# Kernel tuning notes

Measured on AMD Instinct MI355X. Metric: run time of the kernel, lower is better.

Reference implementation:

```python
import jax, jax.numpy as jnp
import numpy as np

B, T, D, N = 2, 2048, 1024, 16
DT_RANK = 64  # ceil(D / 16)


def setup_inputs() -> dict:
    key = jax.random.key(0)
    ks = jax.random.split(key, 8)
    x = jax.random.normal(ks[0], (B, T, D), dtype=jnp.float32)
    # Linear weights stored as (out, in) like torch; applied as x @ W.T
    W_B = jax.random.normal(ks[1], (N, D), dtype=jnp.float32) / np.sqrt(D)
    W_C = jax.random.normal(ks[2], (N, D), dtype=jnp.float32) / np.sqrt(D)
    W_dt1 = jax.random.normal(ks[3], (DT_RANK, D), dtype=jnp.float32) / np.sqrt(D)
    W_dt2 = jax.random.normal(ks[4], (D, DT_RANK), dtype=jnp.float32) / np.sqrt(DT_RANK)
    # dt bias init: inverse-softplus of dt sampled log-uniform in [dt_min, dt_max]
    dt_min, dt_max = 1e-3, 1e-1
    u = jax.random.uniform(ks[5], (D,), dtype=jnp.float32)
    dt_init = jnp.clip(jnp.exp(u * (np.log(dt_max) - np.log(dt_min)) + np.log(dt_min)), 1e-4, None)
    b_dt2 = dt_init + jnp.log(-jnp.expm1(-dt_init))
    # log_A: per original non-HiPPO path, A in (0.5, 1.0), broadcast to (D, N)
    a = jax.random.uniform(ks[6], (N,), dtype=jnp.float32) * 0.5 + 0.5
    log_A = jnp.broadcast_to(jnp.log(a)[None, :], (D, N)).copy()
    D_skip = jnp.ones((D,), dtype=jnp.float32)
    return {"x": x, "W_B": W_B, "W_C": W_C, "W_dt1": W_dt1,
            "W_dt2": W_dt2, "b_dt2": b_dt2, "log_A": log_A, "D_skip": D_skip}


def _selective_scan(A_bar, B_bar, C):
    # A_bar, B_bar: (B, T, D, N); C: (B, T, N) -> y: (B, T, D)
    def step(h, inputs):
        a_t, b_t, c_t = inputs  # (B,D,N), (B,D,N), (B,N)
        h = a_t * h + b_t
        y_t = jnp.einsum('bdn,bn->bd', h, c_t)
        return h, y_t

    h0 = jnp.zeros(A_bar.shape[:1] + A_bar.shape[2:], dtype=A_bar.dtype)  # (B,D,N)
    xs = (jnp.moveaxis(A_bar, 1, 0), jnp.moveaxis(B_bar, 1, 0), jnp.moveaxis(C, 1, 0))
    _, ys = jax.lax.scan(step, h0, xs)  # ys: (T, B, D)
    return jnp.moveaxis(ys, 0, 1)


def reference(x, W_B, W_C, W_dt1, W_dt2, b_dt2, log_A, D_skip):
    # Projections
    B_t = jnp.einsum('btd,nd->btn', x, W_B)          # (B,T,N)
    C_t = jnp.einsum('btd,nd->btn', x, W_C)          # (B,T,N)
    dt_raw = jnp.einsum('btr,dr->btd', jnp.einsum('btd,rd->btr', x, W_dt1), W_dt2) + b_dt2
    dt = jax.nn.softplus(dt_raw)                     # (B,T,D)
    A = -jnp.exp(log_A)                              # (D,N), negative
    # Discretization
    A_bar = jnp.exp(dt[..., None] * A[None, None])   # (B,T,D,N)
    dB = (A_bar - 1.0) / (A[None, None] + 1e-8)
    B_bar = dB * x[..., None] * B_t[:, :, None, :]   # (B,T,D,N)
    y = _selective_scan(A_bar, B_bar, C_t)           # (B,T,D)
    return y + D_skip * x
```

## Files before the change

### kernel.cpp

```cpp
#include <hip/hip_runtime.h>
#include <hip/hip_bf16.h>

#define BB 2
#define TT 2048
#define DD 1024
#define NN 16
#define RR 64
#define MM (BB*TT)
#define KDIM DD
#define CHUNK 64
#define NCHUNK (TT/CHUNK)

#define BT_OFF 0
#define CT_OFF 65536
#define R1_OFF 131072
#define DT_OFF 393216
#define P_OFF  4587520
#define S_OFF  5636096

__device__ __forceinline__ float softplus_f(float z) {
    return fmaxf(z, 0.0f) + log1pf(expf(-fabsf(z)));
}

__global__ __launch_bounds__(256) void k_proj96(
    const float* __restrict__ x, const float* __restrict__ W_B,
    const float* __restrict__ W_C, const float* __restrict__ W_dt1,
    float* __restrict__ Bt, float* __restrict__ Ct, float* __restrict__ R1)
{
    __shared__ float xs[16][68];
    __shared__ float wsT[16][97];

    const int tid = threadIdx.x;
    const int r0 = blockIdx.x * 64;
    const int kbase = blockIdx.y * 256;
    const int tx = tid & 15;
    const int ty = tid >> 4;

    float acc[4][6];
    #pragma unroll
    for (int i = 0; i < 4; i++)
        #pragma unroll
        for (int j = 0; j < 6; j++) acc[i][j] = 0.0f;

    for (int kc = 0; kc < 256; kc += 16) {
        {
            const int row = tid >> 2;
            const int kq = (tid & 3) * 4;
            float4 v = *(const float4*)(x + (size_t)(r0 + row) * KDIM + kbase + kc + kq);
            xs[kq + 0][row] = v.x; xs[kq + 1][row] = v.y;
            xs[kq + 2][row] = v.z; xs[kq + 3][row] = v.w;
        }
        #pragma unroll
        for (int i = 0; i < 6; i++) {
            const int idx = i * 256 + tid;
            const int c = idx >> 4;
            const int kk = idx & 15;
            const float* wrow; int cc;
            if (c < 16)      { wrow = W_B;   cc = c; }
            else if (c < 32) { wrow = W_C;   cc = c - 16; }
            else             { wrow = W_dt1; cc = c - 32; }
            wsT[kk][c] = wrow[(size_t)cc * KDIM + kbase + kc + kk];
        }
        __syncthreads();
        #pragma unroll
        for (int kk = 0; kk < 16; kk++) {
            const float a0 = xs[kk][ty * 4 + 0];
            const float a1 = xs[kk][ty * 4 + 1];
            const float a2 = xs[kk][ty * 4 + 2];
            const float a3 = xs[kk][ty * 4 + 3];
            #pragma unroll
            for (int j = 0; j < 6; j++) {
                const float b = wsT[kk][tx + j * 16];
                acc[0][j] = fmaf(a0, b, acc[0][j]);
                acc[1][j] = fmaf(a1, b, acc[1][j]);
                acc[2][j] = fmaf(a2, b, acc[2][j]);
                acc[3][j] = fmaf(a3, b, acc[3][j]);
            }
        }
        __syncthreads();
    }

    #pragma unroll
    for (int i = 0; i < 4; i++) {
        const int r = r0 + ty * 4 + i;
        #pragma unroll
        for (int j = 0; j < 6; j++) {
            const int c = tx + j * 16;
            const float v = acc[i][j];
            if (c < 16)      atomicAdd(&Bt[r * NN + c], v);
            else if (c < 32) atomicAdd(&Ct[r * NN + (c - 16)], v);
            else             atomicAdd(&R1[r * RR + (c - 32)], v);
        }
    }
}

__global__ __launch_bounds__(256) void k_dtproj(
    const float* __restrict__ R1, const float* __restrict__ W_dt2,
    const float* __restrict__ b_dt2, float* __restrict__ dt)
{
    __shared__ float r1s[16][65];
    __shared__ float wsT[64][256];

    const int tid = threadIdx.x;
    const int r0 = blockIdx.x * 16;
    const int d0 = blockIdx.y * 256;

    {
        const int row = tid >> 4;
        const int kq = (tid & 15) * 4;
        float4 v = *(const float4*)(R1 + (size_t)(r0 + row) * RR + kq);
        r1s[row][kq + 0] = v.x; r1s[row][kq + 1] = v.y;
        r1s[row][kq + 2] = v.z; r1s[row][kq + 3] = v.w;
    }
    {
        const float* src = W_dt2 + (size_t)(d0 + tid) * RR;
        #pragma unroll
        for (int kq = 0; kq < 64; kq += 4) {
            float4 v = *(const float4*)(src + kq);
            wsT[kq + 0][tid] = v.x; wsT[kq + 1][tid] = v.y;
            wsT[kq + 2][tid] = v.z; wsT[kq + 3][tid] = v.w;
        }
    }
    __syncthreads();

    const int r = tid & 15;
    const int dg = tid >> 4;

    float4 acc[4];
    #pragma unroll
    for (int q = 0; q < 4; q++) acc[q] = make_float4(0.f, 0.f, 0.f, 0.f);

    #pragma unroll 4
    for (int k = 0; k < 64; k++) {
        const float a = r1s[r][k];
        #pragma unroll
        for (int q = 0; q < 4; q++) {
            float4 bv = *(const float4*)&wsT[k][dg * 16 + q * 4];
            acc[q].x = fmaf(a, bv.x, acc[q].x);
            acc[q].y = fmaf(a, bv.y, acc[q].y);
            acc[q].z = fmaf(a, bv.z, acc[q].z);
            acc[q].w = fmaf(a, bv.w, acc[q].w);
        }
    }

    float* out = dt + (size_t)(r0 + r) * DD + d0 + dg * 16;
    const float* bb = b_dt2 + d0 + dg * 16;
    #pragma unroll
    for (int q = 0; q < 4; q++) {
        float4 bias = *(const float4*)(bb + q * 4);
        float4 o;
        o.x = softplus_f(acc[q].x + bias.x);
        o.y = softplus_f(acc[q].y + bias.y);
        o.z = softplus_f(acc[q].z + bias.z);
        o.w = softplus_f(acc[q].w + bias.w);
        *(float4*)(out + q * 4) = o;
    }
}

__global__ __launch_bounds__(256) void k_scan1(
    const float* __restrict__ x, const float* __restrict__ dt,
    const float* __restrict__ Bt, const float* __restrict__ log_A,
    float* __restrict__ P, float* __restrict__ S)
{
    __shared__ float dt_s[CHUNK][64];
    __shared__ float x_s[CHUNK][64];
    __shared__ float bt_s[CHUNK][NN];

    const int tid = threadIdx.x;
    const int ng = tid & 3;
    const int dl = tid >> 2;
    const int d0 = blockIdx.x * 64;
    const int d  = d0 + dl;
    const int c  = blockIdx.y;
    const int b  = blockIdx.z;
    const int n0 = ng * 4;
    const int base = b * TT + c * CHUNK;

    {
        const float* gdt = dt + (size_t)base * DD + d0;
        const float* gx  = x  + (size_t)base * DD + d0;
        #pragma unroll
        for (int k = 0; k < 4; k++) {
            const int f = tid + k * 256;
            const int t = f >> 4;
            const int j = (f & 15) * 4;
            *(float4*)&dt_s[t][j] = *(const float4*)(gdt + (size_t)t * DD + j);
            *(float4*)&x_s[t][j]  = *(const float4*)(gx  + (size_t)t * DD + j);
        }
        const float* gbt = Bt + (size_t)base * NN;
        const int t = tid >> 2;
        const int j = (tid & 3) * 4;
        *(float4*)&bt_s[t][j] = *(const float4*)(gbt + (size_t)t * NN + j);
    }

    const float4 lg = *(const float4*)(log_A + d * NN + n0);
    const float A0 = -__expf(lg.x), A1 = -__expf(lg.y),
                A2 = -__expf(lg.z), A3 = -__expf(lg.w);
    const float rA0 = 1.0f / (A0 + 1e-8f), rA1 = 1.0f / (A1 + 1e-8f),
                rA2 = 1.0f / (A2 + 1e-8f), rA3 = 1.0f / (A3 + 1e-8f);

    __syncthreads();

    float P0 = 1.f, P1 = 1.f, P2 = 1.f, P3 = 1.f;
    float S0 = 0.f, S1 = 0.f, S2 = 0.f, S3 = 0.f;

    #pragma unroll 16
    for (int t = 0; t < CHUNK; t++) {
        const float dtv = dt_s[t][dl];
        const float xv  = x_s[t][dl];
        const float4 bt4 = *(const float4*)&bt_s[t][n0];
        const float a0 = __expf(dtv * A0);
        const float a1 = __expf(dtv * A1);
        const float a2 = __expf(dtv * A2);
        const float a3 = __expf(dtv * A3);
        const float u0 = rA0 * xv * bt4.x;
        const float u1 = rA1 * xv * bt4.y;
        const float u2 = rA2 * xv * bt4.z;
        const float u3 = rA3 * xv * bt4.w;
        S0 = fmaf(a0, S0 + u0, -u0);
        S1 = fmaf(a1, S1 + u1, -u1);
        S2 = fmaf(a2, S2 + u2, -u2);
        S3 = fmaf(a3, S3 + u3, -u3);
        P0 *= a0; P1 *= a1; P2 *= a2; P3 *= a3;
    }

    const int oidx = ((c * BB + b) * DD + d) * NN + n0;
    *(float4*)(P + oidx) = make_float4(P0, P1, P2, P3);
    *(float4*)(S + oidx) = make_float4(S0, S1, S2, S3);
}

__global__ __launch_bounds__(256) void k_scan2(
    const float* __restrict__ x, const float* __restrict__ dt,
    const float* __restrict__ Bt, const float* __restrict__ Ct,
    const float* __restrict__ log_A, const float* __restrict__ D_skip,
    const float* __restrict__ P, const float* __restrict__ S,
    float* __restrict__ y)
{
    __shared__ float dt_s[CHUNK][64];
    __shared__ float x_s[CHUNK][64];
    __shared__ float bt_s[CHUNK][NN];
    __shared__ float ct_s[CHUNK][NN];

    const int tid = threadIdx.x;
    const int ng = tid & 3;
    const int dl = tid >> 2;
    const int d0 = blockIdx.x * 64;
    const int d  = d0 + dl;
    const int c  = blockIdx.y;
    const int b  = blockIdx.z;
    const int n0 = ng * 4;
    const int base = b * TT + c * CHUNK;

    {
        const float* gdt = dt + (size_t)base * DD + d0;
        const float* gx  = x  + (size_t)base * DD + d0;
        #pragma unroll
        for (int k = 0; k < 4; k++) {
            const int f = tid + k * 256;
            const int t = f >> 4;
            const int j = (f & 15) * 4;
            *(float4*)&dt_s[t][j] = *(const float4*)(gdt + (size_t)t * DD + j);
            *(float4*)&x_s[t][j]  = *(const float4*)(gx  + (size_t)t * DD + j);
        }
        const float* gbt = Bt + (size_t)base * NN;
        const float* gct = Ct + (size_t)base * NN;
        const int t = tid >> 2;
        const int j = (tid & 3) * 4;
        *(float4*)&bt_s[t][j] = *(const float4*)(gbt + (size_t)t * NN + j);
        *(float4*)&ct_s[t][j] = *(const float4*)(gct + (size_t)t * NN + j);
    }

    const float4 lg = *(const float4*)(log_A + d * NN + n0);
    const float A0 = -__expf(lg.x), A1 = -__expf(lg.y),
                A2 = -__expf(lg.z), A3 = -__expf(lg.w);
    const float rA0 = 1.0f / (A0 + 1e-8f), rA1 = 1.0f / (A1 + 1e-8f),
                rA2 = 1.0f / (A2 + 1e-8f), rA3 = 1.0f / (A3 + 1e-8f);
    const float dsk = D_skip[d];

    float h0 = 0.f, h1 = 0.f, h2 = 0.f, h3 = 0.f;
    for (int cc = 0; cc < c; cc++) {
        const int idx = ((cc * BB + b) * DD + d) * NN + n0;
        const float4 Pv = *(const float4*)(P + idx);
        const float4 Sv = *(const float4*)(S + idx);
        h0 = fmaf(Pv.x, h0, Sv.x);
        h1 = fmaf(Pv.y, h1, Sv.y);
        h2 = fmaf(Pv.z, h2, Sv.z);
        h3 = fmaf(Pv.w, h3, Sv.w);
    }
    __syncthreads();

    float* yp = y + (size_t)base * DD + d;

    #pragma unroll 16
    for (int t = 0; t < CHUNK; t++) {
        const float dtv = dt_s[t][dl];
        const float xv  = x_s[t][dl];
        const float4 bt4 = *(const float4*)&bt_s[t][n0];
        const float4 ct4 = *(const float4*)&ct_s[t][n0];
        const float a0 = __expf(dtv * A0);
        const float a1 = __expf(dtv * A1);
        const float a2 = __expf(dtv * A2);
        const float a3 = __expf(dtv * A3);
        const float u0 = rA0 * xv * bt4.x;
        const float u1 = rA1 * xv * bt4.y;
        const float u2 = rA2 * xv * bt4.z;
        const float u3 = rA3 * xv * bt4.w;
        h0 = fmaf(a0, h0 + u0, -u0);
        h1 = fmaf(a1, h1 + u1, -u1);
        h2 = fmaf(a2, h2 + u2, -u2);
        h3 = fmaf(a3, h3 + u3, -u3);
        float part = fmaf(h3, ct4.w, fmaf(h2, ct4.z, fmaf(h1, ct4.y, h0 * ct4.x)));
        part += __shfl_xor(part, 1);
        part += __shfl_xor(part, 2);
        if (ng == 0) yp[(size_t)t * DD] = fmaf(dsk, xv, part);
    }
}

extern "C" void kernel_launch(void* const* d_in, const int* in_sizes, int n_in,
                              void* d_out, int out_size, void* d_ws, size_t ws_size,
                              hipStream_t stream)
{
    const float* x      = (const float*)d_in[0];
    const float* W_B    = (const float*)d_in[1];
    const float* W_C    = (const float*)d_in[2];
    const float* W_dt1  = (const float*)d_in[3];
    const float* W_dt2  = (const float*)d_in[4];
    const float* b_dt2  = (const float*)d_in[5];
    const float* log_A  = (const float*)d_in[6];
    const float* D_skip = (const float*)d_in[7];
    float* y = (float*)d_out;

    float* ws = (float*)d_ws;
    float* Bt = ws + BT_OFF;
    float* Ct = ws + CT_OFF;
    float* R1 = ws + R1_OFF;
    float* dt = ws + DT_OFF;
    float* P  = ws + P_OFF;
    float* S  = ws + S_OFF;

    hipMemsetAsync(d_ws, 0, (size_t)DT_OFF * sizeof(float), stream);

    k_proj96<<<dim3(MM / 64, 4), 256, 0, stream>>>(x, W_B, W_C, W_dt1, Bt, Ct, R1);
    k_dtproj<<<dim3(MM / 16, DD / 256), 256, 0, stream>>>(R1, W_dt2, b_dt2, dt);
    k_scan1<<<dim3(DD / 64, NCHUNK, BB), 256, 0, stream>>>(x, dt, Bt, log_A, P, S);
    k_scan2<<<dim3(DD / 64, NCHUNK, BB), 256, 0, stream>>>(x, dt, Bt, Ct, log_A, D_skip, P, S, y);
}
```

Before: 182.1 us.

## Replace split-K atomics with partial buffers and retile dt projection GEMM

The projection kernel now writes split-K partial sums to a workspace buffer instead of using atomicAdd. A new reduction kernel sums the four partials and scatters them into Bt, Ct and R1, which also removes the workspace memset. W_dt2 is pre-transposed by a small kernel so the dt projection can load weights with coalesced float4 reads, and that GEMM is retiled to 64 rows by 256 columns with a 4x16 register tile per thread. This adds two extra launches and extra partial-buffer traffic in exchange for removing atomics and raising arithmetic intensity in the dt GEMM.

Result: faster. 177.4 us (-2.6%).

```diff
diff --git a/kernel.cpp b/kernel.cpp
--- a/kernel.cpp
+++ b/kernel.cpp
@@ -17,15 +17,42 @@
 #define DT_OFF 393216
 #define P_OFF  4587520
 #define S_OFF  5636096
+#define PP_OFF 6684672
+#define WT_OFF 8257536
 
 __device__ __forceinline__ float softplus_f(float z) {
     return fmaxf(z, 0.0f) + log1pf(expf(-fabsf(z)));
+}
+
+__global__ __launch_bounds__(256) void k_wtT(
+    const float* __restrict__ W, float* __restrict__ WT)
+{
+    __shared__ float tile[64][68];
+    const int tid = threadIdx.x;
+    const int d0 = blockIdx.x * 64;
+    #pragma unroll
+    for (int i = 0; i < 4; i++) {
+        const int f = tid + i * 256;
+        const int dr = f >> 4;
+        const int kq = (f & 15) * 4;
+        *(float4*)&tile[dr][kq] = *(const float4*)(W + (size_t)(d0 + dr) * RR + kq);
+    }
+    __syncthreads();
+    #pragma unroll
+    for (int i = 0; i < 4; i++) {
+        const int f = tid + i * 256;
+        const int k = f >> 4;
+        const int dq = (f & 15) * 4;
+        float4 v = make_float4(tile[dq + 0][k], tile[dq + 1][k],
+                               tile[dq + 2][k], tile[dq + 3][k]);
+        *(float4*)(WT + (size_t)k * DD + d0 + dq) = v;
+    }
 }
 
 __global__ __launch_bounds__(256) void k_proj96(
     const float* __restrict__ x, const float* __restrict__ W_B,
     const float* __restrict__ W_C, const float* __restrict__ W_dt1,
-    float* __restrict__ Bt, float* __restrict__ Ct, float* __restrict__ R1)
+    float* __restrict__ Pp)
 {
     __shared__ float xs[16][68];
     __shared__ float wsT[16][97];
@@ -80,80 +107,114 @@
         __syncthreads();
     }
 
+    float* out = Pp + (size_t)blockIdx.y * (MM * 96);
     #pragma unroll
     for (int i = 0; i < 4; i++) {
         const int r = r0 + ty * 4 + i;
         #pragma unroll
-        for (int j = 0; j < 6; j++) {
-            const int c = tx + j * 16;
-            const float v = acc[i][j];
-            if (c < 16)      atomicAdd(&Bt[r * NN + c], v);
-            else if (c < 32) atomicAdd(&Ct[r * NN + (c - 16)], v);
-            else             atomicAdd(&R1[r * RR + (c - 32)], v);
-        }
-    }
+        for (int j = 0; j < 6; j++)
+            out[(size_t)r * 96 + tx + j * 16] = acc[i][j];
+    }
+}
+
+__global__ __launch_bounds__(256) void k_reduce96(
+    const float* __restrict__ Pp, float* __restrict__ Bt,
+    float* __restrict__ Ct, float* __restrict__ R1)
+{
+    const int gid = blockIdx.x * 256 + threadIdx.x;
+    const int e0 = gid * 4;
+    float4 s = *(const float4*)(Pp + e0);
+    const float4 p1 = *(const float4*)(Pp + (size_t)MM * 96 + e0);
+    const float4 p2 = *(const float4*)(Pp + (size_t)2 * MM * 96 + e0);
+    const float4 p3 = *(const float4*)(Pp + (size_t)3 * MM * 96 + e0);
+    s.x += p1.x + p2.x + p3.x;
+    s.y += p1.y + p2.y + p3.y;
+    s.z += p1.z + p2.z + p3.z;
+    s.w += p1.w + p2.w + p3.w;
+    const int r = e0 / 96;
+    const int c = e0 - r * 96;
+    if (c < 16)      *(float4*)(Bt + (size_t)r * NN + c) = s;
+    else if (c < 32) *(float4*)(Ct + (size_t)r * NN + (c - 16)) = s;
+    else             *(float4*)(R1 + (size_t)r * RR + (c - 32)) = s;
 }
 
 __global__ __launch_bounds__(256) void k_dtproj(
-    const float* __restrict__ R1, const float* __restrict__ W_dt2,
+    const float* __restrict__ R1, const float* __restrict__ WT,
     const float* __restrict__ b_dt2, float* __restrict__ dt)
 {
-    __shared__ float r1s[16][65];
+    __shared__ float r1s[64][68];
     __shared__ float wsT[64][256];
 
     const int tid = threadIdx.x;
-    const int r0 = blockIdx.x * 16;
+    const int r0 = blockIdx.x * 64;
     const int d0 = blockIdx.y * 256;
 
-    {
-        const int row = tid >> 4;
-        const int kq = (tid & 15) * 4;
-        float4 v = *(const float4*)(R1 + (size_t)(r0 + row) * RR + kq);
-        r1s[row][kq + 0] = v.x; r1s[row][kq + 1] = v.y;
-        r1s[row][kq + 2] = v.z; r1s[row][kq + 3] = v.w;
-    }
-    {
-        const float* src = W_dt2 + (size_t)(d0 + tid) * RR;
-        #pragma unroll
-        for (int kq = 0; kq < 64; kq += 4) {
-            float4 v = *(const float4*)(src + kq);
-            wsT[kq + 0][tid] = v.x; wsT[kq + 1][tid] = v.y;
-            wsT[kq + 2][tid] = v.z; wsT[kq + 3][tid] = v.w;
-        }
+    #pragma unroll
+    for (int i = 0; i < 4; i++) {
+        const int f = tid + i * 256;
+        const int row = f >> 4;
+        const int kq = (f & 15) * 4;
+        *(float4*)&r1s[row][kq] = *(const float4*)(R1 + (size_t)(r0 + row) * RR + kq);
+    }
+    #pragma unroll
+    for (int i = 0; i < 16; i++) {
+        const int f = tid + i * 256;
+        const int kk = f >> 6;
+        const int dl4 = (f & 63) * 4;
+        *(float4*)&wsT[kk][dl4] = *(const float4*)(WT + (size_t)kk * DD + d0 + dl4);
     }
     __syncthreads();
 
-    const int r = tid & 15;
-    const int dg = tid >> 4;
-
-    float4 acc[4];
-    #pragma unroll
-    for (int q = 0; q < 4; q++) acc[q] = make_float4(0.f, 0.f, 0.f, 0.f);
-
-    #pragma unroll 4
-    for (int k = 0; k < 64; k++) {
-        const float a = r1s[r][k];
-        #pragma unroll
-        for (int q = 0; q < 4; q++) {
-            float4 bv = *(const float4*)&wsT[k][dg * 16 + q * 4];
-            acc[q].x = fmaf(a, bv.x, acc[q].x);
-            acc[q].y = fmaf(a, bv.y, acc[q].y);
-            acc[q].z = fmaf(a, bv.z, acc[q].z);
-            acc[q].w = fmaf(a, bv.w, acc[q].w);
-        }
-    }
-
-    float* out = dt + (size_t)(r0 + r) * DD + d0 + dg * 16;
-    const float* bb = b_dt2 + d0 + dg * 16;
+    const int cg = tid & 15;
+    const int rg = tid >> 4;
+
+    float4 acc[4][4];
+    #pragma unroll
+    for (int i = 0; i < 4; i++)
+        #pragma unroll
+        for (int q = 0; q < 4; q++) acc[i][q] = make_float4(0.f, 0.f, 0.f, 0.f);
+
+    for (int k4 = 0; k4 < 16; k4++) {
+        float r1a[4][4];
+        #pragma unroll
+        for (int i = 0; i < 4; i++) {
+            const float4 v = *(const float4*)&r1s[rg * 4 + i][k4 * 4];
+            r1a[i][0] = v.x; r1a[i][1] = v.y; r1a[i][2] = v.z; r1a[i][3] = v.w;
+        }
+        #pragma unroll
+        for (int kk = 0; kk < 4; kk++) {
+            const int k = k4 * 4 + kk;
+            float4 w[4];
+            #pragma unroll
+            for (int q = 0; q < 4; q++)
+                w[q] = *(const float4*)&wsT[k][q * 64 + cg * 4];
+            #pragma unroll
+            for (int i = 0; i < 4; i++) {
+                const float a = r1a[i][kk];
+                #pragma unroll
+                for (int q = 0; q < 4; q++) {
+                    acc[i][q].x = fmaf(a, w[q].x, acc[i][q].x);
+                    acc[i][q].y = fmaf(a, w[q].y, acc[i][q].y);
+                    acc[i][q].z = fmaf(a, w[q].z, acc[i][q].z);
+                    acc[i][q].w = fmaf(a, w[q].w, acc[i][q].w);
+                }
+            }
+        }
+    }
+
     #pragma unroll
     for (int q = 0; q < 4; q++) {
-        float4 bias = *(const float4*)(bb + q * 4);
-        float4 o;
-        o.x = softplus_f(acc[q].x + bias.x);
-        o.y = softplus_f(acc[q].y + bias.y);
-        o.z = softplus_f(acc[q].z + bias.z);
-        o.w = softplus_f(acc[q].w + bias.w);
-        *(float4*)(out + q * 4) = o;
+        const float4 bias = *(const float4*)(b_dt2 + d0 + q * 64 + cg * 4);
+        #pragma unroll
+        for (int i = 0; i < 4; i++) {
+            const int row = r0 + rg * 4 + i;
+            float4 o;
+            o.x = softplus_f(acc[i][q].x + bias.x);
+            o.y = softplus_f(acc[i][q].y + bias.y);
+            o.z = softplus_f(acc[i][q].z + bias.z);
+            o.w = softplus_f(acc[i][q].w + bias.w);
+            *(float4*)(dt + (size_t)row * DD + d0 + q * 64 + cg * 4) = o;
+        }
     }
 }
 
@@ -337,11 +398,13 @@
     float* dt = ws + DT_OFF;
     float* P  = ws + P_OFF;
     float* S  = ws + S_OFF;
-
-    hipMemsetAsync(d_ws, 0, (size_t)DT_OFF * sizeof(float), stream);
-
-    k_proj96<<<dim3(MM / 64, 4), 256, 0, stream>>>(x, W_B, W_C, W_dt1, Bt, Ct, R1);
-    k_dtproj<<<dim3(MM / 16, DD / 256), 256, 0, stream>>>(R1, W_dt2, b_dt2, dt);
+    float* Pp = ws + PP_OFF;
+    float* WT = ws + WT_OFF;
+
+    k_wtT<<<dim3(DD / 64), 256, 0, stream>>>(W_dt2, WT);
+    k_proj96<<<dim3(MM / 64, 4), 256, 0, stream>>>(x, W_B, W_C, W_dt1, Pp);
+    k_reduce96<<<dim3(MM * 96 / 4 / 256), 256, 0, stream>>>(Pp, Bt, Ct, R1);
+    k_dtproj<<<dim3(MM / 64, DD / 256), 256, 0, stream>>>(R1, WT, b_dt2, dt);
     k_scan1<<<dim3(DD / 64, NCHUNK, BB), 256, 0, stream>>>(x, dt, Bt, log_A, P, S);
     k_scan2<<<dim3(DD / 64, NCHUNK, BB), 256, 0, stream>>>(x, dt, Bt, Ct, log_A, D_skip, P, S, y);
 }
```
